# Performance work log

Hardware: AMD Instinct MI355X
Metric: run time of the kernel (lower is better)

## Reference

```python
import jax, jax.numpy as jnp
import numpy as np

NUM_STEPS = 50
DT = 0.01
COUPLING_STRENGTH = 1.0
TWO_PI = np.float32(2.0 * np.pi)


def setup_inputs() -> dict:
    key = jax.random.key(0)
    k1, k2, k3 = jax.random.split(key, 3)
    B, N, D = 8, 2048, 256
    initial_state = jax.random.uniform(k1, (B, N), dtype=jnp.float32) * 2.0 * np.pi
    embeddings = jax.random.normal(k2, (B, N, D), dtype=jnp.float32)
    omega = jax.random.normal(k3, (N,), dtype=jnp.float32) * 0.1
    return {"initial_state": initial_state, "embeddings": embeddings, "omega": omega}


def _build_coupling(embeddings):
    # cosine similarity, clamped to [0, 1] (F.normalize with eps=1e-12)
    norm = jnp.linalg.norm(embeddings, axis=-1, keepdims=True)
    emb_norm = embeddings / jnp.maximum(norm, 1e-12)
    coupling = jnp.einsum('bnd,bmd->bnm', emb_norm, emb_norm)
    return jnp.clip(coupling, 0.0, None)


def reference(initial_state, embeddings, omega):
    B, N = initial_state.shape
    coupling = _build_coupling(embeddings)  # [B, N, N]
    k_over_n = jnp.float32(COUPLING_STRENGTH / N)
    dt = jnp.float32(DT)

    def step(theta, _):
        # phase_diff[b,i,j] = theta_i - theta_j
        phase_diff = theta[:, :, None] - theta[:, None, :]
        coupling_sum = jnp.einsum('bij,bij->bi', coupling, jnp.sin(phase_diff))
        dtheta = omega + k_over_n * coupling_sum
        theta = jnp.fmod(theta + dt * dtheta, TWO_PI)
        return theta, None

    theta, _ = jax.lax.scan(step, initial_state, None, length=NUM_STEPS)
    return theta
```

## Files before the change

### kernel.cpp

```cpp
#include <hip/hip_runtime.h>
#include <hip/hip_bf16.h>


constexpr int B = 8;
constexpr int N = 2048;
constexpr int D = 256;
constexpr int STEPS = 50;
constexpr int ROWS = 64;
constexpr int BPB  = 32;
constexpr int TPB  = 512;
constexpr float DT = 0.01f;
constexpr float K_OVER_N = 1.0f / 2048.0f;
constexpr float TWO_PI_F = 6.2831854820251465f;

using bf16x8 = __attribute__((ext_vector_type(8))) short;
using f32x4  = __attribute__((ext_vector_type(4))) float;

static __device__ __forceinline__ unsigned short f2bf(float f) {
    union { float f; unsigned int i; } v; v.f = f;
    unsigned int x = v.i;
    x += 0x7fffu + ((x >> 16) & 1u);
    return (unsigned short)(x >> 16);
}
static __device__ __forceinline__ unsigned char f2fp8(float f) {
    return (unsigned char)(__builtin_amdgcn_cvt_pk_fp8_f32(f, f, 0, false) & 0xff);
}

__global__ void normalize_k(const float* __restrict__ emb,
                            unsigned short* __restrict__ En) {
    const int row  = blockIdx.x * 4 + (threadIdx.x >> 6);
    const int lane = threadIdx.x & 63;
    const float4 v = *(const float4*)(emb + (size_t)row * D + lane * 4);
    float ss = v.x * v.x + v.y * v.y + v.z * v.z + v.w * v.w;
    #pragma unroll
    for (int k = 32; k >= 1; k >>= 1) ss += __shfl_xor(ss, k);
    const float inv = 1.0f / fmaxf(sqrtf(ss), 1e-12f);
    ushort4 o;
    o.x = f2bf(v.x * inv); o.y = f2bf(v.y * inv);
    o.z = f2bf(v.z * inv); o.w = f2bf(v.w * inv);
    *(ushort4*)(En + (size_t)row * D + lane * 4) = o;
}

__global__ __launch_bounds__(512, 2) void fused_steps_k(
        const unsigned short* __restrict__ En,
        const float* __restrict__ theta0,
        float* __restrict__ out,
        const float* __restrict__ omega,
        unsigned int* __restrict__ msg) {
    __shared__ unsigned char s_C[ROWS * 2048];
    __shared__ unsigned char s_tbl[2080 + 2048];
    __shared__ f32x4 s_acc[8][8];

    const int b  = blockIdx.x;
    const int rt = blockIdx.y;
    const int t  = threadIdx.x;
    const int w = t >> 6, lane = t & 63;
    const int col = lane & 15, g = lane >> 4;
    const int grp = w >> 1, kh = w & 1;

    float th = 0.f, sth = 0.f, cth = 0.f, om = 0.f;
    if (t < ROWS) {
        th = theta0[(size_t)b * N + rt * ROWS + t];
        om = omega[rt * ROWS + t];
        sth = __sinf(th); cth = __cosf(th);
        const unsigned int m = (1u << 16) |
            ((unsigned int)f2fp8(sth) << 8) | (unsigned int)f2fp8(cth);
        __hip_atomic_store(&msg[(size_t)b * N + rt * ROWS + t], m,
                           __ATOMIC_RELAXED, __HIP_MEMORY_SCOPE_AGENT);
    }

    {
        const unsigned short* EnB = En + (size_t)b * N * D;
        const int fr = lane & 15;
        const int fq = lane >> 4;
        bf16x8 bf[4][8];
        #pragma unroll
        for (int gi = 0; gi < 4; ++gi)
            #pragma unroll
            for (int kc = 0; kc < 8; ++kc)
                bf[gi][kc] = *(const bf16x8*)(EnB +
                    (size_t)(rt * ROWS + gi * 16 + fr) * D + kc * 32 + fq * 8);
        for (int jt = w * 16; jt < w * 16 + 16; ++jt) {
            f32x4 acc[4];
            #pragma unroll
            for (int gi = 0; gi < 4; ++gi)
                acc[gi] = (f32x4){0.f, 0.f, 0.f, 0.f};
            #pragma unroll
            for (int kc = 0; kc < 8; ++kc) {
                const bf16x8 A = *(const bf16x8*)(EnB +
                    (size_t)(jt * 16 + fr) * D + kc * 32 + fq * 8);
                #pragma unroll
                for (int gi = 0; gi < 4; ++gi)
                    acc[gi] = __builtin_amdgcn_mfma_f32_16x16x32_bf16(A, bf[gi][kc], acc[gi], 0, 0, 0);
            }
            #pragma unroll
            for (int gi = 0; gi < 4; ++gi) {
                int wpk = __builtin_amdgcn_cvt_pk_fp8_f32(fmaxf(acc[gi][0], 0.f),
                                                          fmaxf(acc[gi][1], 0.f), 0, false);
                wpk = __builtin_amdgcn_cvt_pk_fp8_f32(fmaxf(acc[gi][2], 0.f),
                                                      fmaxf(acc[gi][3], 0.f), wpk, true);
                const int io = gi * 16 + fr;
                const int jb = jt * 16 + fq * 4;
                *(unsigned int*)(s_C + io * 2048 + (jb ^ ((io & 7) << 4))) = (unsigned int)wpk;
            }
        }
    }
    __syncthreads();

    const unsigned char* Abase = s_C + (grp * 16 + col) * 2048;
    const unsigned int sw = (unsigned)((col & 7) << 4);
    const int tblbase = (col == 1) ? 2080 : 0;
    const int o0 = kh * 1024 + g * 8;
    const int r0 = t * 4;

    for (int s = 0; s < STEPS; ++s) {
        const unsigned int* mb = msg + ((size_t)(s & 1) * B + b) * N + r0;
        const unsigned int tgt = (unsigned int)(s + 1);
        unsigned int g0, g1, g2, g3;
        for (;;) {
            g0 = __hip_atomic_load(mb + 0, __ATOMIC_RELAXED, __HIP_MEMORY_SCOPE_AGENT);
            g1 = __hip_atomic_load(mb + 1, __ATOMIC_RELAXED, __HIP_MEMORY_SCOPE_AGENT);
            g2 = __hip_atomic_load(mb + 2, __ATOMIC_RELAXED, __HIP_MEMORY_SCOPE_AGENT);
            g3 = __hip_atomic_load(mb + 3, __ATOMIC_RELAXED, __HIP_MEMORY_SCOPE_AGENT);
            if (((g0 >> 16) == tgt) & ((g1 >> 16) == tgt) &
                ((g2 >> 16) == tgt) & ((g3 >> 16) == tgt)) break;
            __builtin_amdgcn_s_sleep(1);
        }
        const unsigned int uc = (g0 & 0xffu) | ((g1 & 0xffu) << 8) |
                                ((g2 & 0xffu) << 16) | ((g3 & 0xffu) << 24);
        const unsigned int us = ((g0 >> 8) & 0xffu) | (((g1 >> 8) & 0xffu) << 8) |
                                (((g2 >> 8) & 0xffu) << 16) | (((g3 >> 8) & 0xffu) << 24);
        *(unsigned int*)(s_tbl + r0) = uc;
        *(unsigned int*)(s_tbl + 2080 + r0) = us;
        __syncthreads();

        f32x4 acc0 = {0.f, 0.f, 0.f, 0.f}, acc1 = {0.f, 0.f, 0.f, 0.f};
        #pragma unroll
        for (int u = 0; u < 32; u += 2) {
            const int oa = o0 + u * 32;
            const long a0 = *(const long*)(Abase + (oa ^ sw));
            const long a1 = *(const long*)(Abase + ((oa + 32) ^ sw));
            long b0 = *(const long*)(s_tbl + tblbase + oa);
            long b1 = *(const long*)(s_tbl + tblbase + oa + 32);
            b0 = (col < 2) ? b0 : 0L;
            b1 = (col < 2) ? b1 : 0L;
            acc0 = __builtin_amdgcn_mfma_f32_16x16x32_fp8_fp8(a0, b0, acc0, 0, 0, 0);
            acc1 = __builtin_amdgcn_mfma_f32_16x16x32_fp8_fp8(a1, b1, acc1, 0, 0, 0);
        }
        acc0 += acc1;
        if (col < 2) s_acc[w][g * 2 + col] = acc0;
        __syncthreads();

        if (t < ROWS) {
            const int gr = t >> 4;
            const int gg = ((t & 15) >> 2) * 2;
            const int rr = t & 3;
            float S1 = 0.f, S2 = 0.f;
            #pragma unroll
            for (int h = 0; h < 2; ++h) {
                S1 += s_acc[gr * 2 + h][gg + 0][rr];
                S2 += s_acc[gr * 2 + h][gg + 1][rr];
            }
            const float csum = sth * S1 - cth * S2;
            th = th + DT * (om + K_OVER_N * csum);
            if (th >= TWO_PI_F) th -= TWO_PI_F;
            if (s < STEPS - 1) {
                sth = __sinf(th); cth = __cosf(th);
                const unsigned int m = ((unsigned int)(s + 2) << 16) |
                    ((unsigned int)f2fp8(sth) << 8) | (unsigned int)f2fp8(cth);
                __hip_atomic_store(
                    &msg[((size_t)((s + 1) & 1) * B + b) * N + rt * ROWS + t],
                    m, __ATOMIC_RELAXED, __HIP_MEMORY_SCOPE_AGENT);
            } else {
                out[(size_t)b * N + rt * ROWS + t] = th;
            }
        }
    }
}

extern "C" void kernel_launch(void* const* d_in, const int* in_sizes, int n_in,
                              void* d_out, int out_size, void* d_ws, size_t ws_size,
                              hipStream_t stream) {
    const float* theta0 = (const float*)d_in[0];
    const float* emb    = (const float*)d_in[1];
    const float* omega  = (const float*)d_in[2];
    float* out = (float*)d_out;

    unsigned short* En = (unsigned short*)d_ws;
    unsigned int*  msg = (unsigned int*)(En + (size_t)B * N * D);

    normalize_k<<<B * N / 4, 256, 0, stream>>>(emb, En);

    fused_steps_k<<<dim3(B, BPB), TPB, 0, stream>>>(En, theta0, out, omega, msg);
}
```

Before: 206.8 us.

## Stage B-tile rows in LDS and split coupling GEMM to cut register pressure

The coupling-build GEMM no longer keeps all 64 B-rows' fragments in registers (32 bf16x8 vectors per lane). Rows 0-47 are staged into the tail of the shared fp8 coupling buffer (the area of rows 48-63, filled later) and read from LDS. Rows 48-63 stay in registers and are handled in a second pass, with the A fragments batch-loaded up front. The aim is lower VGPR pressure and better latency hiding in the prologue, at the cost of extra LDS reads, a second pass that re-reads A from global, and added barriers.

Result: slower. 229.3 us (+10.9%).

```diff
diff --git a/kernel.cpp b/kernel.cpp
--- a/kernel.cpp
+++ b/kernel.cpp
@@ -73,28 +73,43 @@
         const unsigned short* EnB = En + (size_t)b * N * D;
         const int fr = lane & 15;
         const int fq = lane >> 4;
-        bf16x8 bf[4][8];
+
+        bf16x8 breg[8];
         #pragma unroll
-        for (int gi = 0; gi < 4; ++gi)
-            #pragma unroll
-            for (int kc = 0; kc < 8; ++kc)
-                bf[gi][kc] = *(const bf16x8*)(EnB +
-                    (size_t)(rt * ROWS + gi * 16 + fr) * D + kc * 32 + fq * 8);
+        for (int kc = 0; kc < 8; ++kc)
+            breg[kc] = *(const bf16x8*)(EnB +
+                (size_t)(rt * ROWS + 48 + fr) * D + kc * 32 + fq * 8);
+
+        #pragma unroll
+        for (int it = 0; it < 3; ++it) {
+            const int L = it * TPB + t;
+            const int r = L >> 5, u = L & 31;
+            *(uint4*)(s_C + 98304 + r * 512 + ((u * 16) ^ ((r & 7) << 4))) =
+                *(const uint4*)((const unsigned char*)(EnB +
+                    (size_t)(rt * ROWS + r) * D) + u * 16);
+        }
+        __syncthreads();
+
         for (int jt = w * 16; jt < w * 16 + 16; ++jt) {
-            f32x4 acc[4];
-            #pragma unroll
-            for (int gi = 0; gi < 4; ++gi)
-                acc[gi] = (f32x4){0.f, 0.f, 0.f, 0.f};
-            #pragma unroll
-            for (int kc = 0; kc < 8; ++kc) {
-                const bf16x8 A = *(const bf16x8*)(EnB +
+            bf16x8 a[8];
+            #pragma unroll
+            for (int kc = 0; kc < 8; ++kc)
+                a[kc] = *(const bf16x8*)(EnB +
                     (size_t)(jt * 16 + fr) * D + kc * 32 + fq * 8);
+            f32x4 acc[3];
+            #pragma unroll
+            for (int gi = 0; gi < 3; ++gi) acc[gi] = (f32x4){0.f, 0.f, 0.f, 0.f};
+            #pragma unroll
+            for (int kc = 0; kc < 8; ++kc)
                 #pragma unroll
-                for (int gi = 0; gi < 4; ++gi)
-                    acc[gi] = __builtin_amdgcn_mfma_f32_16x16x32_bf16(A, bf[gi][kc], acc[gi], 0, 0, 0);
-            }
-            #pragma unroll
-            for (int gi = 0; gi < 4; ++gi) {
+                for (int gi = 0; gi < 3; ++gi) {
+                    const int r = gi * 16 + fr;
+                    const bf16x8 bb = *(const bf16x8*)(s_C + 98304 + r * 512 +
+                        ((kc * 64 + fq * 16) ^ ((r & 7) << 4)));
+                    acc[gi] = __builtin_amdgcn_mfma_f32_16x16x32_bf16(a[kc], bb, acc[gi], 0, 0, 0);
+                }
+            #pragma unroll
+            for (int gi = 0; gi < 3; ++gi) {
                 int wpk = __builtin_amdgcn_cvt_pk_fp8_f32(fmaxf(acc[gi][0], 0.f),
                                                           fmaxf(acc[gi][1], 0.f), 0, false);
                 wpk = __builtin_amdgcn_cvt_pk_fp8_f32(fmaxf(acc[gi][2], 0.f),
@@ -103,6 +118,26 @@
                 const int jb = jt * 16 + fq * 4;
                 *(unsigned int*)(s_C + io * 2048 + (jb ^ ((io & 7) << 4))) = (unsigned int)wpk;
             }
+        }
+        __syncthreads();
+
+        for (int jt = w * 16; jt < w * 16 + 16; ++jt) {
+            bf16x8 a[8];
+            #pragma unroll
+            for (int kc = 0; kc < 8; ++kc)
+                a[kc] = *(const bf16x8*)(EnB +
+                    (size_t)(jt * 16 + fr) * D + kc * 32 + fq * 8);
+            f32x4 acc = {0.f, 0.f, 0.f, 0.f};
+            #pragma unroll
+            for (int kc = 0; kc < 8; ++kc)
+                acc = __builtin_amdgcn_mfma_f32_16x16x32_bf16(a[kc], breg[kc], acc, 0, 0, 0);
+            int wpk = __builtin_amdgcn_cvt_pk_fp8_f32(fmaxf(acc[0], 0.f),
+                                                      fmaxf(acc[1], 0.f), 0, false);
+            wpk = __builtin_amdgcn_cvt_pk_fp8_f32(fmaxf(acc[2], 0.f),
+                                                  fmaxf(acc[3], 0.f), wpk, true);
+            const int io = 48 + fr;
+            const int jb = jt * 16 + fq * 4;
+            *(unsigned int*)(s_C + io * 2048 + (jb ^ ((io & 7) << 4))) = (unsigned int)wpk;
         }
     }
     __syncthreads();
```
